# Performance work log

Measured on AMD Instinct MI355X. Metric: run time of the kernel, lower is better.

The kernel has to match this reference:

```python
import jax, jax.numpy as jnp
import numpy as np

B, T, H = 16, 64, 256  # batch, timesteps (= num stacked layers), hidden
L = T                  # MultiRNNCell([cell]*timesteps): layers == timesteps, shared weights


def setup_inputs() -> dict:
    key = jax.random.key(0)
    k1, k2, k3 = jax.random.split(key, 3)
    x = jax.random.normal(k1, (B, T, H), dtype=jnp.float32)
    init_state = jax.random.normal(k2, (L, 2, B, H), dtype=jnp.float32) * 0.1  # [L, (c,h), B, H]
    W = jax.random.normal(k3, (2 * H, 4 * H), dtype=jnp.float32) / np.sqrt(2 * H)
    b = jnp.zeros((4 * H,), dtype=jnp.float32)
    return {"x": x, "init_state": init_state, "W": W, "b": b}


def reference(x, init_state, W, b):
    # TF LSTMCell math: gates order (i, j, f, o), forget_bias = 1.0
    c0 = init_state[:, 0]  # [L,B,H]
    h0 = init_state[:, 1]  # [L,B,H]

    def layer_fn(inp, st):
        # inp: [B,H] input to this layer; st = (c,h) each [B,H]
        lc, lh = st
        z = jnp.concatenate([inp, lh], axis=-1) @ W + b  # [B,4H]
        i, j, f, o = jnp.split(z, 4, axis=-1)
        nc = jax.nn.sigmoid(f + 1.0) * lc + jax.nn.sigmoid(i) * jnp.tanh(j)
        nh = jax.nn.sigmoid(o) * jnp.tanh(nc)
        return nh, (nc, nh)  # carry = input to next layer; ys = new per-layer state

    def step(carry, xt):
        # carry: (c,h) each [L,B,H]; xt: [B,H]
        c, h = carry
        top_h, (nc, nh) = jax.lax.scan(layer_fn, xt, (c, h))
        return (nc, nh), top_h

    (_, _), ys = jax.lax.scan(step, (c0, h0), jnp.transpose(x, (1, 0, 2)))  # ys: [T,B,H]
    return jnp.transpose(ys, (1, 0, 2))  # [B,T,H] top-layer outputs (dynamic_rnn outputs)
```

## Files before the change

### kernel.cpp

```cpp
#include <hip/hip_runtime.h>

typedef _Float16 half8 __attribute__((ext_vector_type(8)));
typedef float f32x4 __attribute__((ext_vector_type(4)));

#define SC_AGENT __HIP_MEMORY_SCOPE_AGENT
#define SC_WG    __HIP_MEMORY_SCOPE_WORKGROUP

constexpr size_t OFF_PROG = 0;
constexpr size_t OFF_H    = 65536;
constexpr size_t SLOT_STRIDE = (size_t)64 * 16 * 128;

__device__ __forceinline__ size_t Widx(int l, int b, int wi) {
  return ((size_t)l * 16 + b) * 128 + wi;
}
__device__ __forceinline__ int wgid(int l, int r) {
  return (((l & 7) * 4 + r) << 3) | (l >> 3);
}
__device__ __forceinline__ float sigm(float v) { return 1.0f / (1.0f + __expf(-v)); }
__device__ __forceinline__ float tanh_(float v) { return 1.0f - 2.0f / (__expf(2.0f * v) + 1.0f); }

__global__ void init_ws(const float* __restrict__ init_state, char* ws) {
  int* prog = (int*)(ws + OFF_PROG);
  unsigned long long* Hw = (unsigned long long*)(ws + OFF_H);
  const int tid = blockIdx.x * 256 + threadIdx.x;
  if (tid < 256) prog[tid] = -1;
  for (int e = tid; e < 64 * 16 * 128; e += 65536) {
    const int wi = e & 127, b = (e >> 7) & 15, l = e >> 11;
    Hw[Widx(l, b, wi)] = 0xFFFE00000000ULL;
    union { _Float16 f; unsigned short s; } h0, h1;
    h0.f = (_Float16)init_state[((l * 2 + 1) * 16 + b) * 256 + 2 * wi];
    h1.f = (_Float16)init_state[((l * 2 + 1) * 16 + b) * 256 + 2 * wi + 1];
    Hw[SLOT_STRIDE + Widx(l, b, wi)] =
        (unsigned long long)h0.s | ((unsigned long long)h1.s << 16) | (0xFFFFULL << 32);
  }
}

__global__ __launch_bounds__(256, 1) void lstm_mfma(
    const float* __restrict__ x, const float* __restrict__ init_state,
    const float* __restrict__ W, const float* __restrict__ bias,
    float* __restrict__ out, char* ws) {
  int* prog = (int*)(ws + OFF_PROG);
  unsigned long long* Hw = (unsigned long long*)(ws + OFF_H);

  const int tid = threadIdx.x;
  const int wg = blockIdx.x;
  const int l = ((wg & 7) << 3) | (wg >> 5);
  const int r = (wg >> 3) & 3;
  const int wv = tid >> 6, lane = tid & 63;

  __shared__ alignas(16) _Float16 aLds[16 * 64 * 8];
  __shared__ alignas(16) float zLds[16 * 260];
  __shared__ unsigned short hLds[16 * 64];

  half8 wreg[64];
#pragma unroll
  for (int q = 0; q < 4; ++q) {
    const int nl = (wv * 4 + q) * 16 + (lane & 15);
    const int col = (nl & 3) * 256 + r * 64 + (nl >> 2);
#pragma unroll
    for (int kb = 0; kb < 16; ++kb) {
      const int k0 = kb * 32 + (lane >> 4) * 8;
      const float* src = W + (size_t)k0 * 1024 + col;
      half8 hv;
#pragma unroll
      for (int jj = 0; jj < 8; ++jj) hv[jj] = (_Float16)src[(size_t)jj * 1024];
      wreg[q * 16 + kb] = hv;
    }
  }

  const int hu = tid & 63, b4 = tid >> 6;
  const int gu = r * 64 + hu;
  float creg[4];
#pragma unroll
  for (int bb = 0; bb < 4; ++bb)
    creg[bb] = init_state[((l * 2 + 0) * 16 + (b4 * 4 + bb)) * 256 + gu];
  const float bi_ = bias[0 * 256 + gu], bj_ = bias[1 * 256 + gu];
  const float bf_ = bias[2 * 256 + gu], bo_ = bias[3 * 256 + gu];

  int kbA[4], lnA[4];
  size_t wbase[4];
#pragma unroll
  for (int i = 0; i < 4; ++i) {
    const int e = i * 256 + tid, kb = e >> 6, ln = e & 63;
    const int m = ln & 15, k0 = kb * 32 + (ln >> 4) * 8;
    kbA[i] = kb; lnA[i] = ln;
    wbase[i] = (i < 2) ? (l > 0 ? Widx(l - 1, m, k0 >> 1) : 0)
                       : Widx(l, m, (k0 - 256) >> 1);
  }

  int* const progIn = &prog[wgid(l > 0 ? l - 1 : 0, r)];
  int* const bpp0 = &prog[wgid(l < 63 ? l + 1 : 63, 0)];
  int* const bpp1 = &prog[wgid(l < 63 ? l + 1 : 63, 1)];
  int* const bpp2 = &prog[wgid(l < 63 ? l + 1 : 63, 2)];
  int* const bpp3 = &prog[wgid(l < 63 ? l + 1 : 63, 3)];

  for (int t = 0; t < 64; ++t) {
    const int slotCur = t & 1, slotPrev = (t + 1) & 1;
    const unsigned short tagIn = (unsigned short)t;
    const unsigned short tagOwn = (unsigned short)(t - 1);

    if (l == 0) {
#pragma unroll
      for (int i = 0; i < 2; ++i) {
        const int kb = kbA[i], ln = lnA[i];
        const int m = ln & 15, k0 = kb * 32 + (ln >> 4) * 8;
        const float* xs = x + ((size_t)m * 64 + t) * 256 + k0;
        half8 hv;
#pragma unroll
        for (int jj = 0; jj < 8; ++jj) hv[jj] = (_Float16)xs[jj];
        *(half8*)&aLds[(size_t)(kb * 64 + ln) * 8] = hv;
      }
    }

    unsigned pend = (l == 0) ? 0xFF00u : 0xFFFFu;
    bool bp = !(tid == 0 && l < 63 && t >= 2);
    int round = 0;
    while (pend || !bp) {
      const bool esc = (round & 1) != 0;
      bool damp = false;
      if (round >= 8 && l > 0 && (pend & 0x00FFu)) {
        int pl = ((round & 7) == 1)
                     ? __hip_atomic_load(progIn, __ATOMIC_RELAXED, SC_AGENT)
                     : __hip_atomic_load(progIn, __ATOMIC_RELAXED, SC_WG);
        damp = (pl < t);
      }
      if (pend && !damp) {
        unsigned long long wv_[16];
#pragma unroll
        for (int i = 0; i < 4; ++i) {
          const unsigned long long* sp =
              Hw + ((i < 2 ? slotCur : slotPrev) ? SLOT_STRIDE : 0) + wbase[i];
#pragma unroll
          for (int j = 0; j < 4; ++j) {
            const int b_ = i * 4 + j;
            if ((pend >> b_) & 1u)
              wv_[b_] = esc ? __hip_atomic_load(sp + j, __ATOMIC_RELAXED, SC_AGENT)
                            : __hip_atomic_load(sp + j, __ATOMIC_RELAXED, SC_WG);
          }
        }
#pragma unroll
        for (int i = 0; i < 4; ++i) {
          unsigned* dp = (unsigned*)&aLds[(size_t)(kbA[i] * 64 + lnA[i]) * 8];
          const unsigned short exp_ = (i < 2) ? tagIn : tagOwn;
#pragma unroll
          for (int j = 0; j < 4; ++j) {
            const int b_ = i * 4 + j;
            if ((pend >> b_) & 1u) {
              const unsigned long long wd = wv_[b_];
              if ((unsigned short)(wd >> 32) == exp_) {
                dp[j] = (unsigned)wd;
                pend &= ~(1u << b_);
              }
            }
          }
        }
      }
      if (!bp) {
        const int need = t - 2;
        int p0, p1, p2, p3;
        if (esc) {
          p0 = __hip_atomic_load(bpp0, __ATOMIC_RELAXED, SC_AGENT);
          p1 = __hip_atomic_load(bpp1, __ATOMIC_RELAXED, SC_AGENT);
          p2 = __hip_atomic_load(bpp2, __ATOMIC_RELAXED, SC_AGENT);
          p3 = __hip_atomic_load(bpp3, __ATOMIC_RELAXED, SC_AGENT);
        } else {
          p0 = __hip_atomic_load(bpp0, __ATOMIC_RELAXED, SC_WG);
          p1 = __hip_atomic_load(bpp1, __ATOMIC_RELAXED, SC_WG);
          p2 = __hip_atomic_load(bpp2, __ATOMIC_RELAXED, SC_WG);
          p3 = __hip_atomic_load(bpp3, __ATOMIC_RELAXED, SC_WG);
        }
        bp = (p0 >= need) && (p1 >= need) && (p2 >= need) && (p3 >= need);
      }
      if (pend || !bp) {
        ++round;
        if (round > 2000000) break;
        if (damp) __builtin_amdgcn_s_sleep(4);
      }
    }
    __syncthreads();
    if (tid == 0) __hip_atomic_store(&prog[wg], t, __ATOMIC_RELAXED, SC_AGENT);

    f32x4 acc[4] = {{0.f, 0.f, 0.f, 0.f}, {0.f, 0.f, 0.f, 0.f},
                    {0.f, 0.f, 0.f, 0.f}, {0.f, 0.f, 0.f, 0.f}};
#pragma unroll
    for (int kb = 0; kb < 16; ++kb) {
      half8 a = *(const half8*)&aLds[(kb * 64 + lane) * 8];
#pragma unroll
      for (int q = 0; q < 4; ++q)
        acc[q] = __builtin_amdgcn_mfma_f32_16x16x32_f16(a, wreg[q * 16 + kb], acc[q], 0, 0, 0);
    }

#pragma unroll
    for (int q = 0; q < 4; ++q) {
      const int nl = (wv * 4 + q) * 16 + (lane & 15);
      const int m0 = (lane >> 4) * 4;
#pragma unroll
      for (int rg = 0; rg < 4; ++rg) zLds[(m0 + rg) * 260 + nl] = acc[q][rg];
    }
    __syncthreads();

#pragma unroll
    for (int bb = 0; bb < 4; ++bb) {
      const int b = b4 * 4 + bb;
      f32x4 zg = *(const f32x4*)&zLds[b * 260 + hu * 4];
      const float iv = zg[0] + bi_, jv = zg[1] + bj_;
      const float fv = zg[2] + bf_, ov = zg[3] + bo_;
      const float nc = sigm(fv + 1.0f) * creg[bb] + sigm(iv) * tanh_(jv);
      const float nh = sigm(ov) * tanh_(nc);
      creg[bb] = nc;
      union { _Float16 f; unsigned short s; } cv;
      cv.f = (_Float16)nh;
      hLds[b * 64 + hu] = cv.s;
      if (l == 63) out[((size_t)b * 64 + t) * 256 + gu] = nh;
    }
    __syncthreads();

    {
      const int b = tid >> 4, lw0 = (tid & 15) * 2;
#pragma unroll
      for (int q = 0; q < 2; ++q) {
        const int lw = lw0 + q, u0 = 2 * lw;
        unsigned lo = (unsigned)hLds[b * 64 + u0] | ((unsigned)hLds[b * 64 + u0 + 1] << 16);
        unsigned long long wd =
            (unsigned long long)lo | ((unsigned long long)tagIn << 32);
        __hip_atomic_store(Hw + (slotCur ? SLOT_STRIDE : 0) + Widx(l, b, r * 32 + lw),
                           wd, __ATOMIC_RELAXED, SC_AGENT);
      }
    }
  }
}

extern "C" void kernel_launch(void* const* d_in, const int* in_sizes, int n_in,
                              void* d_out, int out_size, void* d_ws,
                              size_t ws_size, hipStream_t stream) {
  const float* x          = (const float*)d_in[0];
  const float* init_state = (const float*)d_in[1];
  const float* W          = (const float*)d_in[2];
  const float* bias       = (const float*)d_in[3];
  float* out = (float*)d_out;
  char* ws   = (char*)d_ws;

  init_ws<<<256, 256, 0, stream>>>(init_state, ws);
  lstm_mfma<<<256, 256, 0, stream>>>(x, init_state, W, bias, out, ws);
}
```

Before: 797.1 us.

## Vectorize tagged-state polling loads and publish hidden state via lane shuffles

Replaces the per-word polling of tagged hidden-state words with wide dwordx4 inline-asm loads (sc0) plus a periodic agent-scope scalar fallback, and drops the upstream-progress damping logic in favor of a short periodic sleep. The hidden-state publish no longer goes through an LDS buffer and an extra __syncthreads; adjacent lanes swap packed fp16 halves with __shfl_xor and even lanes store the tagged 64-bit words directly. The aim is lower latency on the inter-workgroup handoff chain. The cost is reliance on sc0 cache behaviour for coherence and the risk of more polling traffic once damping is removed.

```diff
diff --git a/kernel.cpp b/kernel.cpp
--- a/kernel.cpp
+++ b/kernel.cpp
@@ -2,9 +2,9 @@
 
 typedef _Float16 half8 __attribute__((ext_vector_type(8)));
 typedef float f32x4 __attribute__((ext_vector_type(4)));
+typedef unsigned int u32x4 __attribute__((ext_vector_type(4)));
 
 #define SC_AGENT __HIP_MEMORY_SCOPE_AGENT
-#define SC_WG    __HIP_MEMORY_SCOPE_WORKGROUP
 
 constexpr size_t OFF_PROG = 0;
 constexpr size_t OFF_H    = 65536;
@@ -50,7 +50,6 @@
 
   __shared__ alignas(16) _Float16 aLds[16 * 64 * 8];
   __shared__ alignas(16) float zLds[16 * 260];
-  __shared__ unsigned short hLds[16 * 64];
 
   half8 wreg[64];
 #pragma unroll
@@ -88,7 +87,6 @@
                        : Widx(l, m, (k0 - 256) >> 1);
   }
 
-  int* const progIn = &prog[wgid(l > 0 ? l - 1 : 0, r)];
   int* const bpp0 = &prog[wgid(l < 63 ? l + 1 : 63, 0)];
   int* const bpp1 = &prog[wgid(l < 63 ? l + 1 : 63, 1)];
   int* const bpp2 = &prog[wgid(l < 63 ? l + 1 : 63, 2)];
@@ -96,8 +94,8 @@
 
   for (int t = 0; t < 64; ++t) {
     const int slotCur = t & 1, slotPrev = (t + 1) & 1;
-    const unsigned short tagIn = (unsigned short)t;
-    const unsigned short tagOwn = (unsigned short)(t - 1);
+    const unsigned expIn = (unsigned)(unsigned short)t;
+    const unsigned expOwn = (unsigned)(unsigned short)(t - 1);
 
     if (l == 0) {
 #pragma unroll
@@ -116,40 +114,56 @@
     bool bp = !(tid == 0 && l < 63 && t >= 2);
     int round = 0;
     while (pend || !bp) {
-      const bool esc = (round & 1) != 0;
-      bool damp = false;
-      if (round >= 8 && l > 0 && (pend & 0x00FFu)) {
-        int pl = ((round & 7) == 1)
-                     ? __hip_atomic_load(progIn, __ATOMIC_RELAXED, SC_AGENT)
-                     : __hip_atomic_load(progIn, __ATOMIC_RELAXED, SC_WG);
-        damp = (pl < t);
-      }
-      if (pend && !damp) {
-        unsigned long long wv_[16];
-#pragma unroll
-        for (int i = 0; i < 4; ++i) {
-          const unsigned long long* sp =
-              Hw + ((i < 2 ? slotCur : slotPrev) ? SLOT_STRIDE : 0) + wbase[i];
-#pragma unroll
-          for (int j = 0; j < 4; ++j) {
-            const int b_ = i * 4 + j;
-            if ((pend >> b_) & 1u)
-              wv_[b_] = esc ? __hip_atomic_load(sp + j, __ATOMIC_RELAXED, SC_AGENT)
-                            : __hip_atomic_load(sp + j, __ATOMIC_RELAXED, SC_WG);
+      if (pend) {
+        if ((round & 3) == 3) {
+#pragma unroll
+          for (int i = 0; i < 4; ++i) {
+            const unsigned long long* sp =
+                Hw + ((i < 2 ? slotCur : slotPrev) ? SLOT_STRIDE : 0) + wbase[i];
+            unsigned* dp = (unsigned*)&aLds[(size_t)(kbA[i] * 64 + lnA[i]) * 8];
+            const unsigned exp_ = (i < 2) ? expIn : expOwn;
+#pragma unroll
+            for (int j = 0; j < 4; ++j) {
+              const int b_ = i * 4 + j;
+              if ((pend >> b_) & 1u) {
+                const unsigned long long wd =
+                    __hip_atomic_load(sp + j, __ATOMIC_RELAXED, SC_AGENT);
+                if ((unsigned)(wd >> 32) == exp_) {
+                  dp[j] = (unsigned)wd;
+                  pend &= ~(1u << b_);
+                }
+              }
+            }
           }
-        }
-#pragma unroll
-        for (int i = 0; i < 4; ++i) {
-          unsigned* dp = (unsigned*)&aLds[(size_t)(kbA[i] * 64 + lnA[i]) * 8];
-          const unsigned short exp_ = (i < 2) ? tagIn : tagOwn;
-#pragma unroll
-          for (int j = 0; j < 4; ++j) {
-            const int b_ = i * 4 + j;
-            if ((pend >> b_) & 1u) {
-              const unsigned long long wd = wv_[b_];
-              if ((unsigned short)(wd >> 32) == exp_) {
-                dp[j] = (unsigned)wd;
-                pend &= ~(1u << b_);
+        } else {
+          u32x4 fv[8];
+#pragma unroll
+          for (int i = 0; i < 4; ++i) {
+            if (!((pend >> (4 * i)) & 0xFu)) continue;
+            const unsigned long long* sp =
+                Hw + ((i < 2 ? slotCur : slotPrev) ? SLOT_STRIDE : 0) + wbase[i];
+            asm volatile("global_load_dwordx4 %0, %1, off sc0"
+                         : "=v"(fv[2 * i]) : "v"(sp));
+            asm volatile("global_load_dwordx4 %0, %1, off sc0"
+                         : "=v"(fv[2 * i + 1]) : "v"(sp + 2));
+          }
+          asm volatile("s_waitcnt vmcnt(0)" ::: "memory");
+          __builtin_amdgcn_sched_barrier(0);
+#pragma unroll
+          for (int i = 0; i < 4; ++i) {
+            unsigned* dp = (unsigned*)&aLds[(size_t)(kbA[i] * 64 + lnA[i]) * 8];
+            const unsigned exp_ = (i < 2) ? expIn : expOwn;
+#pragma unroll
+            for (int j = 0; j < 4; ++j) {
+              const int b_ = i * 4 + j;
+              if ((pend >> b_) & 1u) {
+                const u32x4 va = fv[2 * i + (j >> 1)];
+                const unsigned lo = va[(j & 1) * 2 + 0];
+                const unsigned tg = va[(j & 1) * 2 + 1];
+                if (tg == exp_) {
+                  dp[j] = lo;
+                  pend &= ~(1u << b_);
+                }
               }
             }
           }
@@ -157,24 +171,16 @@
       }
       if (!bp) {
         const int need = t - 2;
-        int p0, p1, p2, p3;
-        if (esc) {
-          p0 = __hip_atomic_load(bpp0, __ATOMIC_RELAXED, SC_AGENT);
-          p1 = __hip_atomic_load(bpp1, __ATOMIC_RELAXED, SC_AGENT);
-          p2 = __hip_atomic_load(bpp2, __ATOMIC_RELAXED, SC_AGENT);
-          p3 = __hip_atomic_load(bpp3, __ATOMIC_RELAXED, SC_AGENT);
-        } else {
-          p0 = __hip_atomic_load(bpp0, __ATOMIC_RELAXED, SC_WG);
-          p1 = __hip_atomic_load(bpp1, __ATOMIC_RELAXED, SC_WG);
-          p2 = __hip_atomic_load(bpp2, __ATOMIC_RELAXED, SC_WG);
-          p3 = __hip_atomic_load(bpp3, __ATOMIC_RELAXED, SC_WG);
-        }
+        int p0 = __hip_atomic_load(bpp0, __ATOMIC_RELAXED, SC_AGENT);
+        int p1 = __hip_atomic_load(bpp1, __ATOMIC_RELAXED, SC_AGENT);
+        int p2 = __hip_atomic_load(bpp2, __ATOMIC_RELAXED, SC_AGENT);
+        int p3 = __hip_atomic_load(bpp3, __ATOMIC_RELAXED, SC_AGENT);
         bp = (p0 >= need) && (p1 >= need) && (p2 >= need) && (p3 >= need);
       }
       if (pend || !bp) {
         ++round;
         if (round > 2000000) break;
-        if (damp) __builtin_amdgcn_s_sleep(4);
+        if ((round & 3) == 0) __builtin_amdgcn_s_sleep(1);
       }
     }
     __syncthreads();
@@ -199,32 +205,42 @@
     }
     __syncthreads();
 
+    unsigned short mybits[4];
 #pragma unroll
     for (int bb = 0; bb < 4; ++bb) {
       const int b = b4 * 4 + bb;
       f32x4 zg = *(const f32x4*)&zLds[b * 260 + hu * 4];
       const float iv = zg[0] + bi_, jv = zg[1] + bj_;
-      const float fv = zg[2] + bf_, ov = zg[3] + bo_;
-      const float nc = sigm(fv + 1.0f) * creg[bb] + sigm(iv) * tanh_(jv);
+      const float fv_ = zg[2] + bf_, ov = zg[3] + bo_;
+      const float nc = sigm(fv_ + 1.0f) * creg[bb] + sigm(iv) * tanh_(jv);
       const float nh = sigm(ov) * tanh_(nc);
       creg[bb] = nc;
       union { _Float16 f; unsigned short s; } cv;
       cv.f = (_Float16)nh;
-      hLds[b * 64 + hu] = cv.s;
+      mybits[bb] = cv.s;
       if (l == 63) out[((size_t)b * 64 + t) * 256 + gu] = nh;
     }
-    __syncthreads();
-
     {
-      const int b = tid >> 4, lw0 = (tid & 15) * 2;
-#pragma unroll
-      for (int q = 0; q < 2; ++q) {
-        const int lw = lw0 + q, u0 = 2 * lw;
-        unsigned lo = (unsigned)hLds[b * 64 + u0] | ((unsigned)hLds[b * 64 + u0 + 1] << 16);
-        unsigned long long wd =
-            (unsigned long long)lo | ((unsigned long long)tagIn << 32);
-        __hip_atomic_store(Hw + (slotCur ? SLOT_STRIDE : 0) + Widx(l, b, r * 32 + lw),
-                           wd, __ATOMIC_RELAXED, SC_AGENT);
+      const unsigned p01 = mybits[0] | ((unsigned)mybits[1] << 16);
+      const unsigned p23 = mybits[2] | ((unsigned)mybits[3] << 16);
+      const unsigned q01 = __shfl_xor(p01, 1, 64);
+      const unsigned q23 = __shfl_xor(p23, 1, 64);
+      if (!(hu & 1)) {
+        unsigned long long* dst = Hw + (slotCur ? SLOT_STRIDE : 0) +
+                                  Widx(l, b4 * 4, r * 32 + (hu >> 1));
+        const unsigned long long tg = (unsigned long long)expIn << 32;
+        __hip_atomic_store(dst + 0 * 128,
+            (unsigned long long)((p01 & 0xFFFFu) | (q01 << 16)) | tg,
+            __ATOMIC_RELAXED, SC_AGENT);
+        __hip_atomic_store(dst + 1 * 128,
+            (unsigned long long)((p01 >> 16) | (q01 & 0xFFFF0000u)) | tg,
+            __ATOMIC_RELAXED, SC_AGENT);
+        __hip_atomic_store(dst + 2 * 128,
+            (unsigned long long)((p23 & 0xFFFFu) | (q23 << 16)) | tg,
+            __ATOMIC_RELAXED, SC_AGENT);
+        __hip_atomic_store(dst + 3 * 128,
+            (unsigned long long)((p23 >> 16) | (q23 & 0xFFFF0000u)) | tg,
+            __ATOMIC_RELAXED, SC_AGENT);
       }
     }
   }
```

Result: slower. 920.7 us (+15.5%).
